# Kernel optimization log

Hardware: AMD Instinct MI355X
Metric: run time of the kernel (lower is better)

## Reference

```python
import jax, jax.numpy as jnp
import numpy as np

N, E, ELG = 5000, 50000, 200000      # nodes, edges of g, edges of line graph
NDIM, EDIM, H, L = 512, 512, 8, 2    # hidden sizes, heads, layers
DK = NDIM // H
REL = 128                            # number of relation types
SCALE = float(np.sqrt(DK))


def _ln(x, g, b, eps=1e-5):
    m = x.mean(-1, keepdims=True)
    v = ((x - m) ** 2).mean(-1, keepdims=True)
    return (x - m) * jax.lax.rsqrt(v + eps) * g + b


def _ffn(x, W1, b1, W2, b2, g, b):
    # FFN with residual + layernorm (post-LN transformer FFN)
    return _ln(x + jnp.maximum(x @ W1 + b1, 0.0) @ W2 + b2, g, b)


def _attend(q, k, v, e, src, dst, n_seg):
    # q,k,v: [n_seg, H, DK]; e: optional per-edge feature [Ne, H, DK]
    ks = k[src] if e is None else k[src] + e
    vs = v[src] if e is None else v[src] + e
    # scaled_exp: exp(clamp(score / sqrt(dk), -10, 10))
    score = jnp.exp(jnp.clip((ks * q[dst]).sum(-1) / SCALE, -10.0, 10.0))  # [Ne, H]
    wv = jax.ops.segment_sum(vs * score[..., None], dst, num_segments=n_seg)
    z = jax.ops.segment_sum(score, dst, num_segments=n_seg)
    return wv / z[..., None]  # div_by_z


def setup_inputs() -> dict:
    key = jax.random.key(0)
    keys = iter(jax.random.split(key, 80))
    nxt = lambda: next(keys)

    def nrm(shape, s=0.02):
        return jax.random.normal(nxt(), shape, dtype=jnp.float32) * s

    inp = {}
    inp['x'] = jax.random.normal(nxt(), (N, NDIM), dtype=jnp.float32)
    inp['edge_feat'] = jax.random.randint(nxt(), (E,), 0, REL, dtype=jnp.int32)
    inp['src_ids'] = jax.random.randint(nxt(), (E,), 0, N, dtype=jnp.int32)
    # cover every node / every lg-node so softmax denominators are nonzero
    inp['dst_ids'] = jnp.concatenate([jnp.arange(N, dtype=jnp.int32),
                                      jax.random.randint(nxt(), (E - N,), 0, N, dtype=jnp.int32)])
    inp['lg_src'] = jax.random.randint(nxt(), (ELG,), 0, E, dtype=jnp.int32)
    inp['lg_dst'] = jnp.concatenate([jnp.arange(E, dtype=jnp.int32),
                                     jax.random.randint(nxt(), (ELG - E,), 0, E, dtype=jnp.int32)])
    inp['rel_embed'] = nrm((REL, EDIM), 1.0)
    for p in ['n', 'e']:
        din = NDIM if p == 'n' else EDIM
        inp[p + '_Wq'] = nrm((L, din, NDIM)); inp[p + '_bq'] = jnp.zeros((L, NDIM), jnp.float32)
        inp[p + '_Wk'] = nrm((L, din, NDIM)); inp[p + '_Wv'] = nrm((L, din, NDIM))
        inp[p + '_Wo'] = nrm((L, NDIM, din)); inp[p + '_bo'] = jnp.zeros((L, din), jnp.float32)
        inp[p + '_ln_g'] = jnp.ones((L, din), jnp.float32); inp[p + '_ln_b'] = jnp.zeros((L, din), jnp.float32)
        inp[p + '_f1'] = nrm((L, din, 4 * din)); inp[p + '_fb1'] = jnp.zeros((L, 4 * din), jnp.float32)
        inp[p + '_f2'] = nrm((L, 4 * din, din)); inp[p + '_fb2'] = jnp.zeros((L, din), jnp.float32)
        inp[p + '_fln_g'] = jnp.ones((L, din), jnp.float32); inp[p + '_fln_b'] = jnp.zeros((L, din), jnp.float32)
    return inp


def reference(x, edge_feat, src_ids, dst_ids, lg_src, lg_dst, rel_embed,
              n_Wq, n_bq, n_Wk, n_Wv, n_Wo, n_bo, n_ln_g, n_ln_b,
              n_f1, n_fb1, n_f2, n_fb2, n_fln_g, n_fln_b,
              e_Wq, e_bq, e_Wk, e_Wv, e_Wo, e_bo, e_ln_g, e_ln_b,
              e_f1, e_fb1, e_f2, e_fb2, e_fln_g, e_fln_b):
    lg_x = rel_embed[edge_feat]  # [E, EDIM]
    for i in range(L):
        # ---- node update on g (attention over incoming edges, edge feats added to k,v) ----
        q = (x @ n_Wq[i] + n_bq[i]).reshape(N, H, DK)
        k = (x @ n_Wk[i]).reshape(N, H, DK)
        v = (x @ n_Wv[i]).reshape(N, H, DK)
        e = lg_x.reshape(E, H, DK)  # edim == ndim (relation_share_heads=False)
        o = _attend(q, k, v, e, src_ids, dst_ids, N).reshape(N, NDIM)
        out_x = _ln(x + o @ n_Wo[i] + n_bo[i], n_ln_g[i], n_ln_b[i])
        out_x = _ffn(out_x, n_f1[i], n_fb1[i], n_f2[i], n_fb2[i], n_fln_g[i], n_fln_b[i])
        # ---- edge update on line graph (uses PRE-update node feats; q+=dst, k+=src, v+=src) ----
        src_x = x[src_ids]
        dst_x = x[dst_ids]
        qe = (lg_x @ e_Wq[i] + e_bq[i] + dst_x).reshape(E, H, DK)
        ke = (lg_x @ e_Wk[i] + src_x).reshape(E, H, DK)
        ve = (lg_x @ e_Wv[i] + src_x).reshape(E, H, DK)
        oe = _attend(qe, ke, ve, None, lg_src, lg_dst, E).reshape(E, NDIM)
        out_lg = _ln(lg_x + oe @ e_Wo[i] + e_bo[i], e_ln_g[i], e_ln_b[i])
        out_lg = _ffn(out_lg, e_f1[i], e_fb1[i], e_f2[i], e_fb2[i], e_fln_g[i], e_fln_b[i])
        x, lg_x = out_x, out_lg
    return (x, lg_x)
```

## Files before the change

### kernel.cpp

```cpp
#include <hip/hip_runtime.h>
#include <math.h>

#define NNODES 5000
#define NEDGES 50000
#define NELG   200000
#define DMODEL 512
#define NH     8
#define NLAYERS 2

typedef __bf16 bf16x8 __attribute__((ext_vector_type(8)));
typedef float  f32x4  __attribute__((ext_vector_type(4)));
typedef unsigned short us8v __attribute__((ext_vector_type(8)));
typedef unsigned short us4v __attribute__((ext_vector_type(4)));

__device__ __forceinline__ float b2f(unsigned short u) {
    union { unsigned int i; float f; } c;
    c.i = ((unsigned int)u) << 16;
    return c.f;
}
__device__ __forceinline__ unsigned short f2b(float f) {
    union { float f; unsigned int i; } c;
    c.f = f;
    unsigned int i = c.i;
    return (unsigned short)((i + 0x7fffu + ((i >> 16) & 1u)) >> 16);
}

#define BM 128
#define BN 128
#define BK 32

struct GemmDst {
    unsigned short* C0; unsigned short* C1; unsigned short* C2;
    const unsigned short* a0; const unsigned short* a1; const unsigned short* a2;
    const int* x0; const int* x1; const int* x2;
    const float* b0; const float* b1; const float* b2;
};

__global__ __launch_bounds__(256) void mfma_gemm_kernel(
    const unsigned short* __restrict__ A, const unsigned short* __restrict__ Bt,
    GemmDst P, int M, int K, int N, int secN, int relu)
{
    __shared__ __align__(16) unsigned short ldsA[BM * BK];
    __shared__ __align__(16) unsigned short ldsB[BN * BK];

    const int nbx  = gridDim.x;
    const int nb   = nbx * gridDim.y;
    const int wgid = blockIdx.y * nbx + blockIdx.x;
    const int xcd  = wgid & 7;
    const int ii   = wgid >> 3;
    const int q8   = nb >> 3, r8 = nb & 7;
    const int base = (xcd < r8) ? xcd * (q8 + 1) : r8 * (q8 + 1) + (xcd - r8) * q8;
    const int tl   = base + ii;
    const int rowBase = (tl / nbx) * BM;
    const int colBase = (tl % nbx) * BN;

    const int tid  = threadIdx.x;
    const int lane = tid & 63;
    const int wave = tid >> 6;
    const int quad = lane >> 4;
    const int l16  = lane & 15;
    const int wm = (wave >> 1) * 64;
    const int wn = (wave & 1) * 64;

    const int g0 = tid, g1 = tid + 256;
    const int r0 = g0 >> 2, r1 = g1 >> 2;
    const int c0g = (g0 & 3) ^ ((r0 >> 1) & 3);
    const int c1g = (g1 & 3) ^ ((r1 >> 1) & 3);
    int ra0 = rowBase + r0; if (ra0 > M - 1) ra0 = M - 1;
    int ra1 = rowBase + r1; if (ra1 > M - 1) ra1 = M - 1;
    const unsigned short* gA0 = A + (size_t)ra0 * K + c0g * 8;
    const unsigned short* gA1 = A + (size_t)ra1 * K + c1g * 8;
    const unsigned short* gB0 = Bt + (size_t)(colBase + r0) * K + c0g * 8;
    const unsigned short* gB1 = Bt + (size_t)(colBase + r1) * K + c1g * 8;
    unsigned short* lA0 = ldsA + g0 * 8;
    unsigned short* lA1 = ldsA + g1 * 8;
    unsigned short* lB0 = ldsB + g0 * 8;
    unsigned short* lB1 = ldsB + g1 * 8;

    const int swz = (l16 >> 1) & 3;
    const int ca = (quad ^ swz) * 8;

    const f32x4 zv = {0.f, 0.f, 0.f, 0.f};
    f32x4 acc[4][4];
    #pragma unroll
    for (int i = 0; i < 4; ++i)
        #pragma unroll
        for (int j = 0; j < 4; ++j) acc[i][j] = zv;

    for (int k0 = 0; k0 < K; k0 += BK) {
        __builtin_amdgcn_global_load_lds(
            (const __attribute__((address_space(1))) void*)(gA0 + k0),
            (__attribute__((address_space(3))) void*)lA0, 16, 0, 0);
        __builtin_amdgcn_global_load_lds(
            (const __attribute__((address_space(1))) void*)(gA1 + k0),
            (__attribute__((address_space(3))) void*)lA1, 16, 0, 0);
        __builtin_amdgcn_global_load_lds(
            (const __attribute__((address_space(1))) void*)(gB0 + k0),
            (__attribute__((address_space(3))) void*)lB0, 16, 0, 0);
        __builtin_amdgcn_global_load_lds(
            (const __attribute__((address_space(1))) void*)(gB1 + k0),
            (__attribute__((address_space(3))) void*)lB1, 16, 0, 0);
        __syncthreads();

        bf16x8 af[4], bfr[4];
        #pragma unroll
        for (int i = 0; i < 4; ++i)
            af[i] = *(const bf16x8*)(ldsA + (wm + i * 16 + l16) * BK + ca);
        #pragma unroll
        for (int j = 0; j < 4; ++j)
            bfr[j] = *(const bf16x8*)(ldsB + (wn + j * 16 + l16) * BK + ca);
        #pragma unroll
        for (int i = 0; i < 4; ++i)
            #pragma unroll
            for (int j = 0; j < 4; ++j)
                acc[i][j] = __builtin_amdgcn_mfma_f32_16x16x32_bf16(
                    bfr[j], af[i], acc[i][j], 0, 0, 0);
        __syncthreads();
    }

    const int sec   = colBase / secN;
    const int cbase = colBase - sec * secN;
    unsigned short*       Cs = (sec == 0) ? P.C0 : ((sec == 1) ? P.C1 : P.C2);
    const unsigned short* ad = (sec == 0) ? P.a0 : ((sec == 1) ? P.a1 : P.a2);
    const int*            gx = (sec == 0) ? P.x0 : ((sec == 1) ? P.x1 : P.x2);
    const float*          bs = (sec == 0) ? P.b0 : ((sec == 1) ? P.b1 : P.b2);

    f32x4 b4[4];
    #pragma unroll
    for (int j = 0; j < 4; ++j) {
        const int n0 = cbase + wn + j * 16 + quad * 4;
        b4[j] = bs ? *(const f32x4*)(bs + n0) : zv;
    }

    #pragma unroll
    for (int i = 0; i < 4; ++i) {
        const int row = rowBase + wm + i * 16 + l16;
        if (row >= M) continue;
        const int arow = gx ? gx[row] : row;
        const unsigned short* ar = ad ? ad + (size_t)arow * secN : nullptr;
        unsigned short* crow = Cs + (size_t)row * secN;
        #pragma unroll
        for (int j = 0; j < 4; ++j) {
            const int n0 = cbase + wn + j * 16 + quad * 4;
            f32x4 v = acc[i][j];
            v += b4[j];
            if (ar) {
                const us4v r4 = *(const us4v*)(ar + n0);
                #pragma unroll
                for (int r = 0; r < 4; ++r) v[r] += b2f(r4[r]);
            }
            if (relu) {
                #pragma unroll
                for (int r = 0; r < 4; ++r) v[r] = fmaxf(v[r], 0.0f);
            }
            us4v o4;
            #pragma unroll
            for (int r = 0; r < 4; ++r) o4[r] = f2b(v[r]);
            *(us4v*)(crow + n0) = o4;
        }
    }
}

__global__ __launch_bounds__(256) void transpose_cast_kernel(
    const float* __restrict__ W, unsigned short* __restrict__ Wt, int K, int N)
{
    __shared__ float t[32][33];
    const int n0 = blockIdx.x << 5, k0 = blockIdx.y << 5;
    const int tx = threadIdx.x & 31, ty = threadIdx.x >> 5;
    #pragma unroll
    for (int r = 0; r < 32; r += 8)
        t[ty + r][tx] = W[(size_t)(k0 + ty + r) * N + n0 + tx];
    __syncthreads();
    #pragma unroll
    for (int r = 0; r < 32; r += 8)
        Wt[(size_t)(n0 + ty + r) * K + k0 + tx] = f2b(t[tx][ty + r]);
}

__global__ __launch_bounds__(256) void ln_kernel(
    unsigned short* __restrict__ x, const float* __restrict__ g,
    const float* __restrict__ b, int M)
{
    const int row = blockIdx.x * 4 + (threadIdx.x >> 6);
    if (row >= M) return;
    const int lane = threadIdx.x & 63;
    unsigned short* xr = x + (size_t)row * DMODEL;

    float vals[8];
    float s = 0.f, s2 = 0.f;
    #pragma unroll
    for (int i = 0; i < 8; ++i) {
        const float v = b2f(xr[lane + i * 64]);
        vals[i] = v; s += v; s2 += v * v;
    }
    #pragma unroll
    for (int o = 32; o > 0; o >>= 1) {
        s  += __shfl_down(s, o);
        s2 += __shfl_down(s2, o);
    }
    s  = __shfl(s, 0);
    s2 = __shfl(s2, 0);
    const float m = s * (1.0f / DMODEL);
    const float var = s2 * (1.0f / DMODEL) - m * m;
    const float r = rsqrtf(var + 1e-5f);
    #pragma unroll
    for (int i = 0; i < 8; ++i) {
        const int c = lane + i * 64;
        xr[c] = f2b((vals[i] - m) * r * g[c] + b[c]);
    }
}

__global__ __launch_bounds__(256) void hist_kernel(
    const int* __restrict__ dst, int* __restrict__ cnt, int ne)
{
    const int j = blockIdx.x * 256 + threadIdx.x;
    if (j < ne) atomicAdd(&cnt[dst[j]], 1);
}

__global__ __launch_bounds__(1024) void scan_kernel(
    const int* __restrict__ cnt, int* __restrict__ off,
    int* __restrict__ cur, int n)
{
    __shared__ int part[1024];
    const int t = threadIdx.x;
    const int chunk = (n + 1023) >> 10;
    const int lo = t * chunk;
    int hi = lo + chunk; if (hi > n) hi = n;
    int s = 0;
    for (int i = lo; i < hi; ++i) s += cnt[i];
    part[t] = s;
    __syncthreads();
    #pragma unroll
    for (int o = 1; o < 1024; o <<= 1) {
        int v = (t >= o) ? part[t - o] : 0;
        __syncthreads();
        part[t] += v;
        __syncthreads();
    }
    int base = (t == 0) ? 0 : part[t - 1];
    const int total = part[1023];
    for (int i = lo; i < hi; ++i) {
        const int c = cnt[i];
        off[i] = base; cur[i] = base;
        base += c;
    }
    if (t == 1023) off[n] = total;
}

__global__ __launch_bounds__(256) void scatter_kernel(
    const int* __restrict__ dst, int* __restrict__ cur,
    int* __restrict__ idx, int ne)
{
    const int j = blockIdx.x * 256 + threadIdx.x;
    if (j < ne) {
        const int p = atomicAdd(&cur[dst[j]], 1);
        idx[p] = j;
    }
}

__global__ __launch_bounds__(256) void attend_kernel(
    unsigned short* __restrict__ q,
    const unsigned short* __restrict__ k,
    const unsigned short* __restrict__ v,
    const unsigned short* __restrict__ efeat,
    const int* __restrict__ src,
    const int* __restrict__ off, const int* __restrict__ idx,
    int nseg)
{
    __shared__ float accS[4][DMODEL];
    __shared__ float zS[4][NH];

    const int seg = blockIdx.x;
    if (seg >= nseg) return;
    const int t = threadIdx.x;
    const int wave = t >> 6, lane = t & 63;
    const int c8 = lane * 8;
    unsigned short* qrow = q + (size_t)seg * DMODEL;

    const us8v q8 = *(const us8v*)(qrow + c8);
    float qv[8];
    #pragma unroll
    for (int j = 0; j < 8; ++j) qv[j] = b2f(q8[j]);

    float acc[8] = {0.f, 0.f, 0.f, 0.f, 0.f, 0.f, 0.f, 0.f};
    float zsum = 0.f;
    const int lo = off[seg], hi = off[seg + 1];
    for (int jj = lo + wave; jj < hi; jj += 4) {
        const int e = idx[jj];
        const int s = src[e];
        const us8v k8 = *(const us8v*)(k + (size_t)s * DMODEL + c8);
        const us8v v8 = *(const us8v*)(v + (size_t)s * DMODEL + c8);
        float p = 0.f;
        float vv[8];
        if (efeat) {
            const us8v e8 = *(const us8v*)(efeat + (size_t)e * DMODEL + c8);
            #pragma unroll
            for (int j = 0; j < 8; ++j) {
                const float ef = b2f(e8[j]);
                p = fmaf(b2f(k8[j]) + ef, qv[j], p);
                vv[j] = b2f(v8[j]) + ef;
            }
        } else {
            #pragma unroll
            for (int j = 0; j < 8; ++j) {
                p = fmaf(b2f(k8[j]), qv[j], p);
                vv[j] = b2f(v8[j]);
            }
        }
        p += __shfl_xor(p, 1);
        p += __shfl_xor(p, 2);
        p += __shfl_xor(p, 4);
        float sc = p * 0.125f;
        sc = fminf(fmaxf(sc, -10.0f), 10.0f);
        sc = __expf(sc);
        zsum += sc;
        #pragma unroll
        for (int j = 0; j < 8; ++j) acc[j] = fmaf(sc, vv[j], acc[j]);
    }

    #pragma unroll
    for (int j = 0; j < 8; ++j) accS[wave][c8 + j] = acc[j];
    if ((lane & 7) == 0) zS[wave][lane >> 3] = zsum;
    __syncthreads();

    const int c0 = t * 2;
    const int h = c0 >> 6;
    const float a0 = accS[0][c0] + accS[1][c0] + accS[2][c0] + accS[3][c0];
    const float a1 = accS[0][c0 + 1] + accS[1][c0 + 1] + accS[2][c0 + 1] + accS[3][c0 + 1];
    const float z  = zS[0][h] + zS[1][h] + zS[2][h] + zS[3][h];
    const float rz = 1.0f / z;
    ushort2 o2;
    o2.x = f2b(a0 * rz);
    o2.y = f2b(a1 * rz);
    *(ushort2*)(qrow + c0) = o2;
}

__global__ __launch_bounds__(256) void gather_rel_kernel(
    const float* __restrict__ rel, const int* __restrict__ ef,
    unsigned short* __restrict__ lg)
{
    const int idx = blockIdx.x * 256 + threadIdx.x;
    if (idx >= NEDGES * DMODEL) return;
    const int e = idx >> 9;
    const int col = idx & 511;
    lg[idx] = f2b(rel[(size_t)ef[e] * DMODEL + col]);
}

__global__ __launch_bounds__(256) void cast_f2b_kernel(
    const float* __restrict__ in, unsigned short* __restrict__ out, int n)
{
    const int idx = blockIdx.x * 256 + threadIdx.x;
    if (idx < n) out[idx] = f2b(in[idx]);
}

__global__ __launch_bounds__(256) void cast_b2f_kernel(
    const unsigned short* __restrict__ in, float* __restrict__ out, int n)
{
    const int idx = blockIdx.x * 256 + threadIdx.x;
    if (idx < n) out[idx] = b2f(in[idx]);
}

__global__ __launch_bounds__(256) void zero_kernel(float4* __restrict__ p, int n4)
{
    const int idx = blockIdx.x * 256 + threadIdx.x;
    if (idx < n4) p[idx] = make_float4(0.f, 0.f, 0.f, 0.f);
}

static inline dim3 gemm_grid(int M, int N)
{
    return dim3(N / BN, (M + BM - 1) / BM);
}

static inline void mgemm(hipStream_t st, const unsigned short* A, const unsigned short* Bt,
                         const float* bias, const unsigned short* add, const int* gidx,
                         unsigned short* C, int M, int K, int N, int relu)
{
    GemmDst P = {C, nullptr, nullptr, add, nullptr, nullptr,
                 gidx, nullptr, nullptr, bias, nullptr, nullptr};
    mfma_gemm_kernel<<<gemm_grid(M, N), 256, 0, st>>>(A, Bt, P, M, K, N, N, relu);
}

static inline void mgemm_qkv(hipStream_t st, const unsigned short* A, const unsigned short* Bt,
                             const float* biasQ,
                             const unsigned short* addQ, const int* gxQ,
                             const unsigned short* addKV, const int* gxKV,
                             unsigned short* Cq, unsigned short* Ck, unsigned short* Cv,
                             int M, int K)
{
    GemmDst P = {Cq, Ck, Cv, addQ, addKV, addKV,
                 gxQ, gxKV, gxKV, biasQ, nullptr, nullptr};
    mfma_gemm_kernel<<<gemm_grid(M, 1536), 256, 0, st>>>(A, Bt, P, M, K, 1536, 512, 0);
}

static inline void tcast(hipStream_t st, const float* W, unsigned short* Wt, int K, int N)
{
    dim3 g(N / 32, K / 32);
    transpose_cast_kernel<<<g, 256, 0, st>>>(W, Wt, K, N);
}
static inline void zero(hipStream_t st, void* p, size_t nfloats)
{
    const int n4 = (int)(nfloats / 4);
    zero_kernel<<<(n4 + 255) / 256, 256, 0, st>>>((float4*)p, n4);
}

extern "C" void kernel_launch(void* const* d_in, const int* in_sizes, int n_in,
                              void* d_out, int out_size, void* d_ws, size_t ws_size,
                              hipStream_t stream)
{
    const float* x_in      = (const float*)d_in[0];
    const int*   edge_feat = (const int*)d_in[1];
    const int*   src_ids   = (const int*)d_in[2];
    const int*   dst_ids   = (const int*)d_in[3];
    const int*   lg_src    = (const int*)d_in[4];
    const int*   lg_dst    = (const int*)d_in[5];
    const float* rel_embed = (const float*)d_in[6];

    const float* n_Wq = (const float*)d_in[7];   const float* n_bq = (const float*)d_in[8];
    const float* n_Wk = (const float*)d_in[9];   const float* n_Wv = (const float*)d_in[10];
    const float* n_Wo = (const float*)d_in[11];  const float* n_bo = (const float*)d_in[12];
    const float* n_lg = (const float*)d_in[13];  const float* n_lb = (const float*)d_in[14];
    const float* n_f1 = (const float*)d_in[15];  const float* n_fb1 = (const float*)d_in[16];
    const float* n_f2 = (const float*)d_in[17];  const float* n_fb2 = (const float*)d_in[18];
    const float* n_fg = (const float*)d_in[19];  const float* n_fb = (const float*)d_in[20];

    const float* e_Wq = (const float*)d_in[21];  const float* e_bq = (const float*)d_in[22];
    const float* e_Wk = (const float*)d_in[23];  const float* e_Wv = (const float*)d_in[24];
    const float* e_Wo = (const float*)d_in[25];  const float* e_bo = (const float*)d_in[26];
    const float* e_lg = (const float*)d_in[27];  const float* e_lb = (const float*)d_in[28];
    const float* e_f1 = (const float*)d_in[29];  const float* e_fb1 = (const float*)d_in[30];
    const float* e_f2 = (const float*)d_in[31];  const float* e_fb2 = (const float*)d_in[32];
    const float* e_fg = (const float*)d_in[33];  const float* e_fb = (const float*)d_in[34];

    const int XSZ  = NNODES * DMODEL;
    const int LGSZ = NEDGES * DMODEL;

    char* ws = (char*)d_ws;
    unsigned short* lg16  = (unsigned short*)(ws);
    unsigned short* ve16  = (unsigned short*)(ws + 51200000);
    int* n_off = (int*)(ws + 102400000);
    int* n_cur = (int*)(ws + 102420480);
    int* n_idx = (int*)(ws + 102440960);
    int* e_off = (int*)(ws + 102641664);
    int* e_cur = (int*)(ws + 102842368);
    int* e_idx = (int*)(ws + 103043072);
    unsigned short* xbufA = (unsigned short*)(ws + 110400000);
    unsigned short* xbufB = (unsigned short*)(ws + 115520000);

    char* ob = (char*)d_out;
    unsigned short* qe16 = (unsigned short*)(ob);
    unsigned short* ke16 = (unsigned short*)(ob + 51200000);
    unsigned short* nq16 = (unsigned short*)(ob);
    unsigned short* nk16 = (unsigned short*)(ob + 5120000);
    unsigned short* nv16 = (unsigned short*)(ob + 10240000);
    unsigned short* nhid = (unsigned short*)(ob);
    unsigned short* wtq  = (unsigned short*)(ob + 102400000);
    unsigned short* wtk  = (unsigned short*)(ob + 102924288);
    unsigned short* wtv  = (unsigned short*)(ob + 103448576);
    unsigned short* wto  = (unsigned short*)(ob + 103972864);
    unsigned short* wtf1 = (unsigned short*)(ob + 104497152);
    unsigned short* wtf2 = (unsigned short*)(ob + 106594304);

    cast_f2b_kernel<<<(XSZ + 255) / 256, 256, 0, stream>>>(x_in, xbufA, XSZ);
    gather_rel_kernel<<<(LGSZ + 255) / 256, 256, 0, stream>>>(rel_embed, edge_feat, lg16);

    zero(stream, n_cur, NNODES);
    zero(stream, e_cur, NEDGES);
    hist_kernel<<<(NEDGES + 255) / 256, 256, 0, stream>>>(dst_ids, n_cur, NEDGES);
    hist_kernel<<<(NELG + 255) / 256, 256, 0, stream>>>(lg_dst, e_cur, NELG);
    scan_kernel<<<1, 1024, 0, stream>>>(n_cur, n_off, n_cur, NNODES);
    scan_kernel<<<1, 1024, 0, stream>>>(e_cur, e_off, e_cur, NEDGES);
    scatter_kernel<<<(NEDGES + 255) / 256, 256, 0, stream>>>(dst_ids, n_cur, n_idx, NEDGES);
    scatter_kernel<<<(NELG + 255) / 256, 256, 0, stream>>>(lg_dst, e_cur, e_idx, NELG);

    unsigned short* xc = xbufA;
    unsigned short* xn = xbufB;

    for (int i = 0; i < NLAYERS; ++i) {
        const size_t wo  = (size_t)i * DMODEL * DMODEL;
        const size_t bo_ = (size_t)i * DMODEL;
        const size_t f1o = (size_t)i * DMODEL * 4 * DMODEL;
        const size_t b1o = (size_t)i * 4 * DMODEL;
        const size_t f2o = (size_t)i * 4 * DMODEL * DMODEL;

        tcast(stream, n_Wq + wo, wtq, 512, 512);
        tcast(stream, n_Wk + wo, wtk, 512, 512);
        tcast(stream, n_Wv + wo, wtv, 512, 512);
        tcast(stream, n_Wo + wo, wto, 512, 512);
        tcast(stream, n_f1 + f1o, wtf1, 512, 2048);
        tcast(stream, n_f2 + f2o, wtf2, 2048, 512);

        mgemm_qkv(stream, xc, wtq, n_bq + bo_,
                  nullptr, nullptr, nullptr, nullptr,
                  nq16, nk16, nv16, NNODES, 512);

        attend_kernel<<<NNODES, 256, 0, stream>>>(
            nq16, nk16, nv16, lg16, src_ids, n_off, n_idx, NNODES);

        mgemm(stream, nq16, wto, n_bo + bo_, xc, nullptr, xn, NNODES, 512, 512, 0);
        ln_kernel<<<(NNODES + 3) / 4, 256, 0, stream>>>(xn, n_lg + bo_, n_lb + bo_, NNODES);
        mgemm(stream, xn, wtf1, n_fb1 + b1o, nullptr, nullptr, nhid, NNODES, 512, 2048, 1);
        mgemm(stream, nhid, wtf2, n_fb2 + bo_, xn, nullptr, xn, NNODES, 2048, 512, 0);
        ln_kernel<<<(NNODES + 3) / 4, 256, 0, stream>>>(xn, n_fg + bo_, n_fb + bo_, NNODES);

        tcast(stream, e_Wq + wo, wtq, 512, 512);
        tcast(stream, e_Wk + wo, wtk, 512, 512);
        tcast(stream, e_Wv + wo, wtv, 512, 512);
        tcast(stream, e_Wo + wo, wto, 512, 512);

        mgemm_qkv(stream, lg16, wtq, e_bq + bo_,
                  xc, dst_ids, xc, src_ids,
                  qe16, ke16, ve16, NEDGES, 512);

        attend_kernel<<<NEDGES, 256, 0, stream>>>(
            qe16, ke16, ve16, nullptr, lg_src, e_off, e_idx, NEDGES);

        mgemm(stream, qe16, wto, e_bo + bo_, lg16, nullptr, lg16, NEDGES, 512, 512, 0);
        ln_kernel<<<(NEDGES + 3) / 4, 256, 0, stream>>>(lg16, e_lg + bo_, e_lb + bo_, NEDGES);

        tcast(stream, e_f1 + f1o, wtf1, 512, 2048);
        tcast(stream, e_f2 + f2o, wtf2, 2048, 512);
        for (int c = 0; c < 4; ++c) {
            unsigned short* y1c = lg16 + (size_t)c * 12500 * DMODEL;
            mgemm(stream, y1c, wtf1, e_fb1 + b1o, nullptr, nullptr, ve16, 12500, 512, 2048, 1);
            mgemm(stream, ve16, wtf2, e_fb2 + bo_, y1c, nullptr, y1c, 12500, 2048, 512, 0);
        }
        ln_kernel<<<(NEDGES + 3) / 4, 256, 0, stream>>>(lg16, e_fg + bo_, e_fb + bo_, NEDGES);

        unsigned short* t = xc; xc = xn; xn = t;
    }

    float* out_f = (float*)d_out;
    cast_b2f_kernel<<<(XSZ + 255) / 256, 256, 0, stream>>>(xc, out_f, XSZ);
    cast_b2f_kernel<<<(LGSZ + 255) / 256, 256, 0, stream>>>(lg16, out_f + XSZ, LGSZ);
}
```

Baseline: 2.329 ms.

## Add 256x256 double-buffered MFMA GEMM for edge GEMMs; one wave per attention segment

Adds a new 512-thread GEMM kernel with 256x256x64 tiles, a two-stage LDS double buffer fed by global_load_lds, and explicit waitcnt/barrier scheduling. It is used for the large edge-side QKV, output-projection and FFN GEMMs, to raise data reuse per tile and overlap loads with MFMA work. The attention kernel is also changed to give each segment a single wave instead of a whole block, which removes the LDS reduction and the barrier. The cost is that high-degree segments are now processed serially by one wave. The larger tiles also waste more work on M tails and put more pressure on registers and LDS.

```diff
diff --git a/kernel.cpp b/kernel.cpp
--- a/kernel.cpp
+++ b/kernel.cpp
@@ -25,16 +25,16 @@
     return (unsigned short)((i + 0x7fffu + ((i >> 16) & 1u)) >> 16);
 }
 
-#define BM 128
-#define BN 128
-#define BK 32
-
 struct GemmDst {
     unsigned short* C0; unsigned short* C1; unsigned short* C2;
     const unsigned short* a0; const unsigned short* a1; const unsigned short* a2;
     const int* x0; const int* x1; const int* x2;
     const float* b0; const float* b1; const float* b2;
 };
+
+#define BM 128
+#define BN 128
+#define BK 32
 
 __global__ __launch_bounds__(256) void mfma_gemm_kernel(
     const unsigned short* __restrict__ A, const unsigned short* __restrict__ Bt,
@@ -161,6 +161,174 @@
     }
 }
 
+#define TM 256
+#define TN 256
+#define TK 64
+
+__global__ __launch_bounds__(512, 2) void mfma_gemm256_kernel(
+    const unsigned short* __restrict__ A, const unsigned short* __restrict__ Bt,
+    GemmDst P, int M, int K, int N, int secN, int relu)
+{
+    __shared__ __align__(16) unsigned short ldsA[2][TM * TK];
+    __shared__ __align__(16) unsigned short ldsB[2][TN * TK];
+
+    const int nbx  = gridDim.x;
+    const int nb   = nbx * gridDim.y;
+    const int wgid = blockIdx.y * nbx + blockIdx.x;
+    const int xcd  = wgid & 7;
+    const int ii   = wgid >> 3;
+    const int q8   = nb >> 3, r8 = nb & 7;
+    const int base = (xcd < r8) ? xcd * (q8 + 1) : r8 * (q8 + 1) + (xcd - r8) * q8;
+    const int tl   = base + ii;
+    const int rowBase = (tl / nbx) * TM;
+    const int colBase = (tl % nbx) * TN;
+
+    const int tid  = threadIdx.x;
+    const int lane = tid & 63;
+    const int wave = tid >> 6;
+    const int quad = lane >> 4;
+    const int l16  = lane & 15;
+    const int wr   = wave >> 2;
+    const int wc   = wave & 3;
+
+    const unsigned short* srcA[4];
+    const unsigned short* srcB[4];
+    int ldsOff[4];
+    #pragma unroll
+    for (int j = 0; j < 4; ++j) {
+        const int p = j * 512 + tid;
+        const int r = p >> 3;
+        const int c = (p & 7) ^ (r & 7);
+        ldsOff[j] = p * 8;
+        int rA = rowBase + r; if (rA > M - 1) rA = M - 1;
+        srcA[j] = A + (size_t)rA * K + c * 8;
+        srcB[j] = Bt + (size_t)(colBase + r) * K + c * 8;
+    }
+
+    const int ca0 = (quad       ^ (l16 & 7)) * 8;
+    const int ca1 = ((quad + 4) ^ (l16 & 7)) * 8;
+    const int aRow0 = wr * 128 + l16;
+    const int bRow0 = wc * 64 + l16;
+
+    const f32x4 zv = {0.f, 0.f, 0.f, 0.f};
+    f32x4 acc[8][4];
+    #pragma unroll
+    for (int i = 0; i < 8; ++i)
+        #pragma unroll
+        for (int j = 0; j < 4; ++j) acc[i][j] = zv;
+
+#define STAGE256(buf, t)                                                      \
+    {                                                                         \
+        unsigned short* dA = ldsA[buf];                                       \
+        unsigned short* dB = ldsB[buf];                                       \
+        const int ko = (t) * TK;                                              \
+        _Pragma("unroll")                                                     \
+        for (int j = 0; j < 4; ++j)                                           \
+            __builtin_amdgcn_global_load_lds(                                 \
+                (const __attribute__((address_space(1))) void*)(srcA[j] + ko),\
+                (__attribute__((address_space(3))) void*)(dA + ldsOff[j]),    \
+                16, 0, 0);                                                    \
+        _Pragma("unroll")                                                     \
+        for (int j = 0; j < 4; ++j)                                           \
+            __builtin_amdgcn_global_load_lds(                                 \
+                (const __attribute__((address_space(1))) void*)(srcB[j] + ko),\
+                (__attribute__((address_space(3))) void*)(dB + ldsOff[j]),    \
+                16, 0, 0);                                                    \
+    }
+
+#define COMPUTE256(buf)                                                       \
+    {                                                                         \
+        const unsigned short* bA = ldsA[buf];                                 \
+        const unsigned short* bB = ldsB[buf];                                 \
+        _Pragma("unroll")                                                     \
+        for (int ks = 0; ks < 2; ++ks) {                                      \
+            const int cs = ks ? ca1 : ca0;                                    \
+            bf16x8 afr[8], bfr[4];                                            \
+            _Pragma("unroll")                                                 \
+            for (int m = 0; m < 8; ++m)                                       \
+                afr[m] = *(const bf16x8*)(bA + (aRow0 + m * 16) * TK + cs);   \
+            _Pragma("unroll")                                                 \
+            for (int n = 0; n < 4; ++n)                                       \
+                bfr[n] = *(const bf16x8*)(bB + (bRow0 + n * 16) * TK + cs);   \
+            _Pragma("unroll")                                                 \
+            for (int m = 0; m < 8; ++m)                                       \
+                _Pragma("unroll")                                             \
+                for (int n = 0; n < 4; ++n)                                   \
+                    acc[m][n] = __builtin_amdgcn_mfma_f32_16x16x32_bf16(      \
+                        bfr[n], afr[m], acc[m][n], 0, 0, 0);                  \
+        }                                                                     \
+    }
+
+    const int nt = K / TK;
+
+    STAGE256(0, 0);
+    STAGE256(1, 1);
+    asm volatile("s_waitcnt vmcnt(8)" ::: "memory");
+    __builtin_amdgcn_s_barrier();
+    __builtin_amdgcn_sched_barrier(0);
+
+    for (int t = 0; t < nt - 2; ++t) {
+        COMPUTE256(t & 1);
+        __builtin_amdgcn_sched_barrier(0);
+        __builtin_amdgcn_s_barrier();
+        STAGE256(t & 1, t + 2);
+        asm volatile("s_waitcnt vmcnt(8)" ::: "memory");
+        __builtin_amdgcn_s_barrier();
+        __builtin_amdgcn_sched_barrier(0);
+    }
+    COMPUTE256(nt & 1);
+    __builtin_amdgcn_sched_barrier(0);
+    asm volatile("s_waitcnt vmcnt(0)" ::: "memory");
+    __builtin_amdgcn_s_barrier();
+    __builtin_amdgcn_sched_barrier(0);
+    COMPUTE256((nt - 1) & 1);
+
+#undef STAGE256
+#undef COMPUTE256
+
+    const int sec   = colBase / secN;
+    const int cbase = colBase - sec * secN;
+    unsigned short*       Cs = (sec == 0) ? P.C0 : ((sec == 1) ? P.C1 : P.C2);
+    const unsigned short* ad = (sec == 0) ? P.a0 : ((sec == 1) ? P.a1 : P.a2);
+    const int*            gx = (sec == 0) ? P.x0 : ((sec == 1) ? P.x1 : P.x2);
+    const float*          bs = (sec == 0) ? P.b0 : ((sec == 1) ? P.b1 : P.b2);
+
+    f32x4 b4[4];
+    #pragma unroll
+    for (int n = 0; n < 4; ++n) {
+        const int n0 = cbase + wc * 64 + n * 16 + quad * 4;
+        b4[n] = bs ? *(const f32x4*)(bs + n0) : zv;
+    }
+
+    #pragma unroll
+    for (int m = 0; m < 8; ++m) {
+        const int row = rowBase + wr * 128 + m * 16 + l16;
+        if (row >= M) continue;
+        const int arow = gx ? gx[row] : row;
+        const unsigned short* ar = ad ? ad + (size_t)arow * secN : nullptr;
+        unsigned short* crow = Cs + (size_t)row * secN;
+        #pragma unroll
+        for (int n = 0; n < 4; ++n) {
+            const int n0 = cbase + wc * 64 + n * 16 + quad * 4;
+            f32x4 v = acc[m][n];
+            v += b4[n];
+            if (ar) {
+                const us4v r4 = *(const us4v*)(ar + n0);
+                #pragma unroll
+                for (int r = 0; r < 4; ++r) v[r] += b2f(r4[r]);
+            }
+            if (relu) {
+                #pragma unroll
+                for (int r = 0; r < 4; ++r) v[r] = fmaxf(v[r], 0.0f);
+            }
+            us4v o4;
+            #pragma unroll
+            for (int r = 0; r < 4; ++r) o4[r] = f2b(v[r]);
+            *(us4v*)(crow + n0) = o4;
+        }
+    }
+}
+
 __global__ __launch_bounds__(256) void transpose_cast_kernel(
     const float* __restrict__ W, unsigned short* __restrict__ Wt, int K, int N)
 {
@@ -266,13 +434,9 @@
     const int* __restrict__ off, const int* __restrict__ idx,
     int nseg)
 {
-    __shared__ float accS[4][DMODEL];
-    __shared__ float zS[4][NH];
-
-    const int seg = blockIdx.x;
+    const int wave = threadIdx.x >> 6, lane = threadIdx.x & 63;
+    const int seg = blockIdx.x * 4 + wave;
     if (seg >= nseg) return;
-    const int t = threadIdx.x;
-    const int wave = t >> 6, lane = t & 63;
     const int c8 = lane * 8;
     unsigned short* qrow = q + (size_t)seg * DMODEL;
 
@@ -284,7 +448,7 @@
     float acc[8] = {0.f, 0.f, 0.f, 0.f, 0.f, 0.f, 0.f, 0.f};
     float zsum = 0.f;
     const int lo = off[seg], hi = off[seg + 1];
-    for (int jj = lo + wave; jj < hi; jj += 4) {
+    for (int jj = lo; jj < hi; ++jj) {
         const int e = idx[jj];
         const int s = src[e];
         const us8v k8 = *(const us8v*)(k + (size_t)s * DMODEL + c8);
@@ -317,21 +481,11 @@
         for (int j = 0; j < 8; ++j) acc[j] = fmaf(sc, vv[j], acc[j]);
     }
 
-    #pragma unroll
-    for (int j = 0; j < 8; ++j) accS[wave][c8 + j] = acc[j];
-    if ((lane & 7) == 0) zS[wave][lane >> 3] = zsum;
-    __syncthreads();
-
-    const int c0 = t * 2;
-    const int h = c0 >> 6;
-    const float a0 = accS[0][c0] + accS[1][c0] + accS[2][c0] + accS[3][c0];
-    const float a1 = accS[0][c0 + 1] + accS[1][c0 + 1] + accS[2][c0 + 1] + accS[3][c0 + 1];
-    const float z  = zS[0][h] + zS[1][h] + zS[2][h] + zS[3][h];
-    const float rz = 1.0f / z;
-    ushort2 o2;
-    o2.x = f2b(a0 * rz);
-    o2.y = f2b(a1 * rz);
-    *(ushort2*)(qrow + c0) = o2;
+    const float rz = 1.0f / zsum;
+    us8v o8;
+    #pragma unroll
+    for (int j = 0; j < 8; ++j) o8[j] = f2b(acc[j] * rz);
+    *(us8v*)(qrow + c8) = o8;
 }
 
 __global__ __launch_bounds__(256) void gather_rel_kernel(
@@ -365,18 +519,14 @@
     if (idx < n4) p[idx] = make_float4(0.f, 0.f, 0.f, 0.f);
 }
 
-static inline dim3 gemm_grid(int M, int N)
-{
-    return dim3(N / BN, (M + BM - 1) / BM);
-}
-
 static inline void mgemm(hipStream_t st, const unsigned short* A, const unsigned short* Bt,
                          const float* bias, const unsigned short* add, const int* gidx,
                          unsigned short* C, int M, int K, int N, int relu)
 {
     GemmDst P = {C, nullptr, nullptr, add, nullptr, nullptr,
                  gidx, nullptr, nullptr, bias, nullptr, nullptr};
-    mfma_gemm_kernel<<<gemm_grid(M, N), 256, 0, st>>>(A, Bt, P, M, K, N, N, relu);
+    dim3 g(N / BN, (M + BM - 1) / BM);
+    mfma_gemm_kernel<<<g, 256, 0, st>>>(A, Bt, P, M, K, N, N, relu);
 }
 
 static inline void mgemm_qkv(hipStream_t st, const unsigned short* A, const unsigned short* Bt,
@@ -388,7 +538,31 @@
 {
     GemmDst P = {Cq, Ck, Cv, addQ, addKV, addKV,
                  gxQ, gxKV, gxKV, biasQ, nullptr, nullptr};
-    mfma_gemm_kernel<<<gemm_grid(M, 1536), 256, 0, st>>>(A, Bt, P, M, K, 1536, 512, 0);
+    dim3 g(1536 / BN, (M + BM - 1) / BM);
+    mfma_gemm_kernel<<<g, 256, 0, st>>>(A, Bt, P, M, K, 1536, 512, 0);
+}
+
+static inline void mgemm256(hipStream_t st, const unsigned short* A, const unsigned short* Bt,
+                            const float* bias, const unsigned short* add, const int* gidx,
+                            unsigned short* C, int M, int K, int N, int relu)
+{
+    GemmDst P = {C, nullptr, nullptr, add, nullptr, nullptr,
+                 gidx, nullptr, nullptr, bias, nullptr, nullptr};
+    dim3 g(N / TN, (M + TM - 1) / TM);
+    mfma_gemm256_kernel<<<g, 512, 0, st>>>(A, Bt, P, M, K, N, N, relu);
+}
+
+static inline void mgemm256_qkv(hipStream_t st, const unsigned short* A, const unsigned short* Bt,
+                                const float* biasQ,
+                                const unsigned short* addQ, const int* gxQ,
+                                const unsigned short* addKV, const int* gxKV,
+                                unsigned short* Cq, unsigned short* Ck, unsigned short* Cv,
+                                int M, int K)
+{
+    GemmDst P = {Cq, Ck, Cv, addQ, addKV, addKV,
+                 gxQ, gxKV, gxKV, biasQ, nullptr, nullptr};
+    dim3 g(1536 / TN, (M + TM - 1) / TM);
+    mfma_gemm256_kernel<<<g, 512, 0, st>>>(A, Bt, P, M, K, 1536, 512, 0);
 }
 
 static inline void tcast(hipStream_t st, const float* W, unsigned short* Wt, int K, int N)
@@ -492,7 +666,7 @@
                   nullptr, nullptr, nullptr, nullptr,
                   nq16, nk16, nv16, NNODES, 512);
 
-        attend_kernel<<<NNODES, 256, 0, stream>>>(
+        attend_kernel<<<(NNODES + 3) / 4, 256, 0, stream>>>(
             nq16, nk16, nv16, lg16, src_ids, n_off, n_idx, NNODES);
 
         mgemm(stream, nq16, wto, n_bo + bo_, xc, nullptr, xn, NNODES, 512, 512, 0);
@@ -506,22 +680,22 @@
         tcast(stream, e_Wv + wo, wtv, 512, 512);
         tcast(stream, e_Wo + wo, wto, 512, 512);
 
-        mgemm_qkv(stream, lg16, wtq, e_bq + bo_,
-                  xc, dst_ids, xc, src_ids,
-                  qe16, ke16, ve16, NEDGES, 512);
-
-        attend_kernel<<<NEDGES, 256, 0, stream>>>(
+        mgemm256_qkv(stream, lg16, wtq, e_bq + bo_,
+                     xc, dst_ids, xc, src_ids,
+                     qe16, ke16, ve16, NEDGES, 512);
+
+        attend_kernel<<<(NEDGES + 3) / 4, 256, 0, stream>>>(
             qe16, ke16, ve16, nullptr, lg_src, e_off, e_idx, NEDGES);
 
-        mgemm(stream, qe16, wto, e_bo + bo_, lg16, nullptr, lg16, NEDGES, 512, 512, 0);
+        mgemm256(stream, qe16, wto, e_bo + bo_, lg16, nullptr, lg16, NEDGES, 512, 512, 0);
         ln_kernel<<<(NEDGES + 3) / 4, 256, 0, stream>>>(lg16, e_lg + bo_, e_lb + bo_, NEDGES);
 
         tcast(stream, e_f1 + f1o, wtf1, 512, 2048);
         tcast(stream, e_f2 + f2o, wtf2, 2048, 512);
         for (int c = 0; c < 4; ++c) {
             unsigned short* y1c = lg16 + (size_t)c * 12500 * DMODEL;
-            mgemm(stream, y1c, wtf1, e_fb1 + b1o, nullptr, nullptr, ve16, 12500, 512, 2048, 1);
-            mgemm(stream, ve16, wtf2, e_fb2 + bo_, y1c, nullptr, y1c, 12500, 2048, 512, 0);
+            mgemm256(stream, y1c, wtf1, e_fb1 + b1o, nullptr, nullptr, ve16, 12500, 512, 2048, 1);
+            mgemm256(stream, ve16, wtf2, e_fb2 + bo_, y1c, nullptr, y1c, 12500, 2048, 512, 0);
         }
         ln_kernel<<<(NEDGES + 3) / 4, 256, 0, stream>>>(lg16, e_fg + bo_, e_fb + bo_, NEDGES);
 
```

Measured after the change: 2.442 ms. 4.8% more time.
